# Kernel optimization log

Measured on AMD Instinct MI355X. Metric: run time of the kernel, lower is better.

## Reference

```python
import jax, jax.numpy as jnp
import numpy as np

K = 3  # kernel_size
P = 1  # padding (must satisfy K == 2*P+1 for the original einsum to be shape-valid)


def setup_inputs() -> dict:
    key = jax.random.key(0)
    k1, k2, k3 = jax.random.split(key, 3)
    b, i, c, L, o = 16, 64, 4, 4096, 64
    x = jax.random.normal(k1, (b, i, c, L), dtype=jnp.float32)
    time_tensor = jax.random.uniform(k2, (b, c, L), dtype=jnp.float32)
    weights = jax.random.normal(k3, (o, i, c, K), dtype=jnp.float32)
    return {"x": x, "time_tensor": time_tensor, "weights": weights}


def reference(x, time_tensor, weights):
    """x: (b,i,c,L), time_tensor: (b,c,L), weights: (o,i,c,K) -> (b,o,c,L).

    Faithful to the torch module: pad x/time by P on the time axis, unfold x
    into sliding windows, pad the unfolded tensor again by P, multiply by the
    time scalar per (b,c,l) and contract over (i,k), then crop P from each end.
    The time factor is scalar per output element, so we factor it out of the
    einsum instead of materializing the (b,o,i,c,k,l) dynamic_weights tensor --
    mathematically identical, massively cheaper.
    """
    xp = jnp.pad(x, ((0, 0), (0, 0), (0, 0), (P, P)))            # (b,i,c,L+2P)
    tp = jnp.pad(time_tensor, ((0, 0), (0, 0), (P, P)))          # (b,c,L+2P)
    Lw = xp.shape[-1] - K + 1                                    # == L since K=2P+1
    # unfold -> (b,i,c,K,Lw), matching torch's permute(0,2,1,4,3) after transpose
    xu = jnp.stack([xp[..., j:j + Lw] for j in range(K)], axis=-2)
    xu = jnp.transpose(xu, (0, 2, 1, 3, 4))                      # (b,c,i,K,Lw)
    xu = jnp.pad(xu, ((0, 0), (0, 0), (0, 0), (0, 0), (P, P)))   # (b,c,i,K,Lw+2P)
    conv = jnp.einsum('oick,bcikl->bocl', weights, xu)           # (b,o,c,L+2P)
    out = conv * tp[:, None, :, :]
    return out[..., P:-P]                                        # (b,o,c,L)
```

## Files before the change

### kernel.cpp

```cpp
#include <hip/hip_runtime.h>


#define NB 16
#define NI 64
#define NC 4
#define NL 4096
#define NO 64
#define KW 3
#define LT 64
#define NT 4
#define LBLK (LT * NT)
#define ROWS (LBLK + 2)
#define ROWB 128
#define TOFF (ROWS * ROWB)
#define LDSB (TOFF + LBLK * 4)

#define W_PACK_BYTES (NO * NI * NC * KW * 2)

typedef float f32x4 __attribute__((ext_vector_type(4)));
typedef short bf16x8 __attribute__((ext_vector_type(8)));
typedef unsigned int u32x2 __attribute__((ext_vector_type(2)));

__device__ inline unsigned short f2bf(float f) {
    unsigned int u = __builtin_bit_cast(unsigned int, f);
    u += 0x7FFFu + ((u >> 16) & 1u);
    return (unsigned short)(u >> 16);
}

__device__ __forceinline__ void block_sync_lds() {
    asm volatile("s_waitcnt lgkmcnt(0)" ::: "memory");
    __builtin_amdgcn_s_barrier();
    asm volatile("" ::: "memory");
}

__global__ __launch_bounds__(256)
void prepack_w_kernel(const float* __restrict__ w, unsigned short* __restrict__ wp) {
    const int idx = blockIdx.x * 256 + threadIdx.x;
    const float v = w[idx];
    const int k = idx % 3;
    int r = idx / 3;
    const int c = r & 3;  r >>= 2;
    const int i = r & 63;
    const int o = r >> 6;
    const int cc   = k * 2 + (i >> 5);
    const int lane = (((i >> 3) & 3) << 4) | (o & 15);
    const int j    = i & 7;
    const int wv   = o >> 4;
    wp[(((c * 4 + wv) * 6 + cc) * 64 + lane) * 8 + j] = f2bf(v);
}

__device__ __forceinline__ void stage_load(const float* __restrict__ xb,
                                           int l0, int g, f32x4 s[4]) {
    const float* p = xb + (size_t)(4 * g) * (NC * NL) + l0;
    s[0] = *(const f32x4*)(p);
    s[1] = *(const f32x4*)(p + NC * NL);
    s[2] = *(const f32x4*)(p + 2 * NC * NL);
    s[3] = *(const f32x4*)(p + 3 * NC * NL);
}

__device__ __forceinline__ void stage_write(char* __restrict__ lds,
                                            int r0, int g, const f32x4 s[4]) {
#pragma unroll
    for (int r = 0; r < 4; ++r) {
        const int rr = r0 + r;
        u32x2 pk;
        pk[0] = (unsigned int)f2bf(s[0][r]) | ((unsigned int)f2bf(s[1][r]) << 16);
        pk[1] = (unsigned int)f2bf(s[2][r]) | ((unsigned int)f2bf(s[3][r]) << 16);
        *(u32x2*)(lds + rr * ROWB + ((8 * g) ^ ((rr & 7) << 4))) = pk;
    }
}

__device__ __forceinline__ void compute_store(const char* __restrict__ lds,
                                              const bf16x8 wfrag[6],
                                              float* __restrict__ ob,
                                              int t, int lb0, int lane) {
    const int lcol  = lane & 15;
    const int ksub2 = (lane >> 4) * 16;

    f32x4 tv[4];
#pragma unroll
    for (int lt = 0; lt < 4; ++lt)
        tv[lt] = *(const f32x4*)(lds + TOFF + 4 * (t * LT + lt * 16 + (lane >> 4) * 4));

    f32x4 acc[4] = {};
#pragma unroll
    for (int lt = 0; lt < 4; ++lt) {
#pragma unroll
        for (int cc = 0; cc < 6; ++cc) {
            const int k    = cc >> 1;
            const int ih   = cc & 1;
            const int row  = t * LT + lt * 16 + lcol + k;
            const int colb = ih * 64 + ksub2;
            const int off  = row * ROWB + (colb ^ ((row & 7) << 4));
            const bf16x8 xf = *(const bf16x8*)(lds + off);
            acc[lt] = __builtin_amdgcn_mfma_f32_16x16x32_bf16(xf, wfrag[cc], acc[lt], 0, 0, 0);
        }
    }
#pragma unroll
    for (int lt = 0; lt < 4; ++lt) {
        const int l0 = lb0 + t * LT + lt * 16 + (lane >> 4) * 4;
        f32x4 r;
#pragma unroll
        for (int q = 0; q < 4; ++q) r[q] = acc[lt][q] * tv[lt][q];
        *(f32x4*)(ob + l0) = r;
    }
}

__global__ __launch_bounds__(256, 4)
void tconv_mfma_kernel(const float* __restrict__ x,
                       const float* __restrict__ tt,
                       const unsigned short* __restrict__ wp,
                       float* __restrict__ out)
{
    __shared__ char lds[LDSB];

    const int t    = threadIdx.x;
    const int lane = t & 63;
    const int wave = t >> 6;
    const int c    = blockIdx.y;
    const int b    = blockIdx.z;
    const int lb0  = blockIdx.x * LBLK;
    const int o0   = wave * 16;
    const int g    = wave * 4 + (lane >> 4);
    const int lq   = 4 * (lane & 15);

    const float* xb = x + ((size_t)b * NI * NC + c) * NL;
    const float* tb = tt + (size_t)(b * NC + c) * NL;
    float* ob = out + ((size_t)b * NO * NC + (size_t)(o0 + (lane & 15)) * NC + c) * NL;

    f32x4 s0[4], s1[4];
    stage_load(xb, lb0 + 0 * LT + lq, g, s0);
    stage_load(xb, lb0 + 1 * LT + lq, g, s1);
    float h = 0.f; int hrow = 0, hcol = 0;
    if (t < 128) {
        const int which = t & 1;
        const int i     = t >> 1;
        hrow = which ? (LBLK + 1) : 0;
        hcol = 2 * i;
        const int lh = which ? (lb0 + LBLK) : (lb0 - 1);
        if (lh >= 0 && lh < NL) h = xb[(size_t)i * (NC * NL) + lh];
    }
    const float tval = tb[lb0 + t];

    bf16x8 wfrag[6];
    {
        const bf16x8* wpb = (const bf16x8*)wp + (size_t)((c * 4 + wave) * 6) * 64 + lane;
#pragma unroll
        for (int cc = 0; cc < 6; ++cc) wfrag[cc] = wpb[cc * 64];
    }

    stage_write(lds, 1 + 0 * LT + lq, g, s0);
    stage_write(lds, 1 + 1 * LT + lq, g, s1);
    if (t < 128)
        *(unsigned short*)(lds + hrow * ROWB + (hcol ^ ((hrow & 7) << 4))) = f2bf(h);
    *(float*)(lds + TOFF + 4 * t) = tval;
    block_sync_lds();

    stage_load(xb, lb0 + 2 * LT + lq, g, s0);
    stage_load(xb, lb0 + 3 * LT + lq, g, s1);

    compute_store(lds, wfrag, ob, 0, lb0, lane);
    stage_write(lds, 1 + 2 * LT + lq, g, s0);
    block_sync_lds();

    compute_store(lds, wfrag, ob, 1, lb0, lane);
    stage_write(lds, 1 + 3 * LT + lq, g, s1);
    block_sync_lds();

    compute_store(lds, wfrag, ob, 2, lb0, lane);
    compute_store(lds, wfrag, ob, 3, lb0, lane);
}

extern "C" void kernel_launch(void* const* d_in, const int* in_sizes, int n_in,
                              void* d_out, int out_size, void* d_ws, size_t ws_size,
                              hipStream_t stream) {
    const float* x  = (const float*)d_in[0];
    const float* tt = (const float*)d_in[1];
    const float* w  = (const float*)d_in[2];
    float* out = (float*)d_out;
    unsigned short* wpck = (unsigned short*)d_ws;

    dim3 block(256);
    prepack_w_kernel<<<dim3(NO * NI * NC * KW / 256), block, 0, stream>>>(w, wpck);

    dim3 grid(NL / LBLK, NC, NB);
    tconv_mfma_kernel<<<grid, block, 0, stream>>>(x, tt, wpck, out);
}
```

Measured before the change: 33.48 us.

## Split waves by length instead of output channel, load all chunks upfront

All four x chunks are now loaded and written to LDS before one barrier, which removes the staged pipeline and two extra barriers. Each wave now computes all 64 output channels for its own 64-wide slice of L instead of 16 channels across all 256 positions. Weight fragments are loaded in two halves and reused with two MFMA accumulators per x fragment, which raises register pressure. The time scale is read straight from global memory rather than staged in LDS. The cost is more live registers for the staged loads and weights, and weight reloads per wave.

```diff
diff --git a/kernel.cpp b/kernel.cpp
--- a/kernel.cpp
+++ b/kernel.cpp
@@ -8,12 +8,11 @@
 #define NO 64
 #define KW 3
 #define LT 64
-#define NT 4
-#define LBLK (LT * NT)
+#define NCH 4
+#define LBLK (LT * NCH)
 #define ROWS (LBLK + 2)
 #define ROWB 128
-#define TOFF (ROWS * ROWB)
-#define LDSB (TOFF + LBLK * 4)
+#define LDSB (ROWS * ROWB)
 
 #define W_PACK_BYTES (NO * NI * NC * KW * 2)
 
@@ -70,42 +69,6 @@
     }
 }
 
-__device__ __forceinline__ void compute_store(const char* __restrict__ lds,
-                                              const bf16x8 wfrag[6],
-                                              float* __restrict__ ob,
-                                              int t, int lb0, int lane) {
-    const int lcol  = lane & 15;
-    const int ksub2 = (lane >> 4) * 16;
-
-    f32x4 tv[4];
-#pragma unroll
-    for (int lt = 0; lt < 4; ++lt)
-        tv[lt] = *(const f32x4*)(lds + TOFF + 4 * (t * LT + lt * 16 + (lane >> 4) * 4));
-
-    f32x4 acc[4] = {};
-#pragma unroll
-    for (int lt = 0; lt < 4; ++lt) {
-#pragma unroll
-        for (int cc = 0; cc < 6; ++cc) {
-            const int k    = cc >> 1;
-            const int ih   = cc & 1;
-            const int row  = t * LT + lt * 16 + lcol + k;
-            const int colb = ih * 64 + ksub2;
-            const int off  = row * ROWB + (colb ^ ((row & 7) << 4));
-            const bf16x8 xf = *(const bf16x8*)(lds + off);
-            acc[lt] = __builtin_amdgcn_mfma_f32_16x16x32_bf16(xf, wfrag[cc], acc[lt], 0, 0, 0);
-        }
-    }
-#pragma unroll
-    for (int lt = 0; lt < 4; ++lt) {
-        const int l0 = lb0 + t * LT + lt * 16 + (lane >> 4) * 4;
-        f32x4 r;
-#pragma unroll
-        for (int q = 0; q < 4; ++q) r[q] = acc[lt][q] * tv[lt][q];
-        *(f32x4*)(ob + l0) = r;
-    }
-}
-
 __global__ __launch_bounds__(256, 4)
 void tconv_mfma_kernel(const float* __restrict__ x,
                        const float* __restrict__ tt,
@@ -120,17 +83,16 @@
     const int c    = blockIdx.y;
     const int b    = blockIdx.z;
     const int lb0  = blockIdx.x * LBLK;
-    const int o0   = wave * 16;
     const int g    = wave * 4 + (lane >> 4);
     const int lq   = 4 * (lane & 15);
 
     const float* xb = x + ((size_t)b * NI * NC + c) * NL;
     const float* tb = tt + (size_t)(b * NC + c) * NL;
-    float* ob = out + ((size_t)b * NO * NC + (size_t)(o0 + (lane & 15)) * NC + c) * NL;
 
-    f32x4 s0[4], s1[4];
-    stage_load(xb, lb0 + 0 * LT + lq, g, s0);
-    stage_load(xb, lb0 + 1 * LT + lq, g, s1);
+    f32x4 s[4][4];
+#pragma unroll
+    for (int ch = 0; ch < NCH; ++ch)
+        stage_load(xb, lb0 + ch * LT + lq, g, s[ch]);
     float h = 0.f; int hrow = 0, hcol = 0;
     if (t < 128) {
         const int which = t & 1;
@@ -140,35 +102,58 @@
         const int lh = which ? (lb0 + LBLK) : (lb0 - 1);
         if (lh >= 0 && lh < NL) h = xb[(size_t)i * (NC * NL) + lh];
     }
-    const float tval = tb[lb0 + t];
 
-    bf16x8 wfrag[6];
-    {
-        const bf16x8* wpb = (const bf16x8*)wp + (size_t)((c * 4 + wave) * 6) * 64 + lane;
 #pragma unroll
-        for (int cc = 0; cc < 6; ++cc) wfrag[cc] = wpb[cc * 64];
-    }
-
-    stage_write(lds, 1 + 0 * LT + lq, g, s0);
-    stage_write(lds, 1 + 1 * LT + lq, g, s1);
+    for (int ch = 0; ch < NCH; ++ch)
+        stage_write(lds, 1 + ch * LT + lq, g, s[ch]);
     if (t < 128)
         *(unsigned short*)(lds + hrow * ROWB + (hcol ^ ((hrow & 7) << 4))) = f2bf(h);
-    *(float*)(lds + TOFF + 4 * t) = tval;
+
     block_sync_lds();
 
-    stage_load(xb, lb0 + 2 * LT + lq, g, s0);
-    stage_load(xb, lb0 + 3 * LT + lq, g, s1);
+    const int lcol  = lane & 15;
+    const int ksub2 = (lane >> 4) * 16;
+    const int rbase = wave * LT;
+    const int lwave = lb0 + wave * LT;
 
-    compute_store(lds, wfrag, ob, 0, lb0, lane);
-    stage_write(lds, 1 + 2 * LT + lq, g, s0);
-    block_sync_lds();
-
-    compute_store(lds, wfrag, ob, 1, lb0, lane);
-    stage_write(lds, 1 + 3 * LT + lq, g, s1);
-    block_sync_lds();
-
-    compute_store(lds, wfrag, ob, 2, lb0, lane);
-    compute_store(lds, wfrag, ob, 3, lb0, lane);
+#pragma unroll
+    for (int hh = 0; hh < 2; ++hh) {
+        bf16x8 wfrag[2][6];
+        {
+            const bf16x8* wpb = (const bf16x8*)wp
+                + (size_t)((c * 4 + 2 * hh) * 6) * 64 + lane;
+#pragma unroll
+            for (int s2 = 0; s2 < 2; ++s2)
+#pragma unroll
+                for (int cc = 0; cc < 6; ++cc)
+                    wfrag[s2][cc] = wpb[(s2 * 6 + cc) * 64];
+        }
+#pragma unroll
+        for (int lt = 0; lt < 4; ++lt) {
+            const int l0 = lwave + lt * 16 + (lane >> 4) * 4;
+            const f32x4 tv = *(const f32x4*)(tb + l0);
+            f32x4 acc[2] = {};
+#pragma unroll
+            for (int cc = 0; cc < 6; ++cc) {
+                const int k   = cc >> 1;
+                const int ih  = cc & 1;
+                const int row = rbase + lt * 16 + lcol + k;
+                const int off = row * ROWB + ((ih * 64 + ksub2) ^ ((row & 7) << 4));
+                const bf16x8 xf = *(const bf16x8*)(lds + off);
+                acc[0] = __builtin_amdgcn_mfma_f32_16x16x32_bf16(xf, wfrag[0][cc], acc[0], 0, 0, 0);
+                acc[1] = __builtin_amdgcn_mfma_f32_16x16x32_bf16(xf, wfrag[1][cc], acc[1], 0, 0, 0);
+            }
+#pragma unroll
+            for (int s2 = 0; s2 < 2; ++s2) {
+                const int o = (2 * hh + s2) * 16 + lcol;
+                float* os = out + ((size_t)b * NO * NC + (size_t)o * NC + c) * NL;
+                f32x4 r;
+#pragma unroll
+                for (int q = 0; q < 4; ++q) r[q] = acc[s2][q] * tv[q];
+                *(f32x4*)(os + l0) = r;
+            }
+        }
+    }
 }
 
 extern "C" void kernel_launch(void* const* d_in, const int* in_sizes, int n_in,
@@ -180,9 +165,8 @@
     float* out = (float*)d_out;
     unsigned short* wpck = (unsigned short*)d_ws;
 
-    dim3 block(256);
-    prepack_w_kernel<<<dim3(NO * NI * NC * KW / 256), block, 0, stream>>>(w, wpck);
+    prepack_w_kernel<<<dim3(NO * NI * NC * KW / 256), dim3(256), 0, stream>>>(w, wpck);
 
     dim3 grid(NL / LBLK, NC, NB);
-    tconv_mfma_kernel<<<grid, block, 0, stream>>>(x, tt, wpck, out);
+    tconv_mfma_kernel<<<grid, dim3(256), 0, stream>>>(x, tt, wpck, out);
 }
```

After: 34.90 us. 4.2% more time.
